# Kernel tuning notes

Measured on AMD Instinct MI355X. Metric: run time of the kernel, lower is better.

The kernel has to match this reference:

```python
import jax, jax.numpy as jnp
import numpy as np

EPS = 1e-5

def _bilinear_sample(xb, ys, xs):
    # xb: [C,H,W]; ys, xs: [H,W] float sample coordinates (zero outside bounds)
    C, H, W = xb.shape
    y0 = jnp.floor(ys); x0 = jnp.floor(xs)
    y1 = y0 + 1.0;      x1 = x0 + 1.0
    wy1 = ys - y0; wy0 = 1.0 - wy1
    wx1 = xs - x0; wx0 = 1.0 - wx1
    def g(yi, xi):
        valid = (yi >= 0) & (yi < H) & (xi >= 0) & (xi < W)
        yc = jnp.clip(yi, 0, H - 1).astype(jnp.int32)
        xc = jnp.clip(xi, 0, W - 1).astype(jnp.int32)
        return xb[:, yc, xc] * valid[None].astype(xb.dtype)  # [C,H,W]
    return (g(y0, x0) * (wy0 * wx0)[None] + g(y0, x1) * (wy0 * wx1)[None]
          + g(y1, x0) * (wy1 * wx0)[None] + g(y1, x1) * (wy1 * wx1)[None])

def _deform_conv2d(x, offset, mask, w, b):
    # x:[B,C,H,W] offset:[B,18,H,W] mask:[B,9,H,W] w:[Co,C,3,3] b:[Co]
    B, C, H, W = x.shape
    Co = w.shape[0]
    ii = jnp.arange(H, dtype=x.dtype)[:, None]
    jj = jnp.arange(W, dtype=x.dtype)[None, :]
    cols = []
    for k in range(9):  # fixed 3x3 kernel positions, row-major (dy=offset[2k], dx=offset[2k+1])
        ky, kx = k // 3 - 1, k % 3 - 1
        ys = ii + ky + offset[:, 2 * k]      # [B,H,W]
        xs = jj + kx + offset[:, 2 * k + 1]
        v = jax.vmap(_bilinear_sample)(x, ys, xs)  # [B,C,H,W]
        cols.append(v * mask[:, k][:, None])
    cols = jnp.stack(cols, axis=1)               # [B,9,C,H,W]
    out = jnp.einsum('bkchw,ock->bohw', cols, w.reshape(Co, C, 9))
    return out + b[None, :, None, None]

def setup_inputs() -> dict:
    key = jax.random.key(0)
    k1, k2, k3, k4 = jax.random.split(key, 4)
    B, Cin, Cout, H, W = 8, 64, 64, 128, 128
    x = jax.random.normal(k1, (B, Cin, H, W), dtype=jnp.float32)
    # offset/mask conv: small weights so learned offsets stay O(1) pixels;
    # bias[18:]=2.0 as in the module's init (masks start near sigmoid(2))
    w_off = jax.random.normal(k2, (27, Cin, 3, 3), dtype=jnp.float32) * 0.01
    b_off = jnp.concatenate([jnp.zeros((18,), jnp.float32), jnp.full((9,), 2.0, jnp.float32)])
    w_dcn = jax.random.normal(k3, (Cout, Cin, 3, 3), dtype=jnp.float32) / np.sqrt(Cin * 9)
    b_dcn = jax.random.normal(k4, (Cout,), dtype=jnp.float32) * 0.01
    return {"x": x, "w_off": w_off, "b_off": b_off, "w_dcn": w_dcn, "b_dcn": b_dcn}

def reference(x, w_off, b_off, w_dcn, b_dcn):
    dn = ('NCHW', 'OIHW', 'NCHW')
    om = jax.lax.conv_general_dilated(x, w_off, (1, 1), 'SAME', dimension_numbers=dn)
    om = om + b_off[None, :, None, None]
    offset = om[:, :18]
    mask = jax.nn.sigmoid(om[:, 18:])
    y = _deform_conv2d(x, offset, mask, w_dcn, b_dcn)
    # InstanceNorm2d (affine=False, biased variance) + ReLU
    mu = jnp.mean(y, axis=(2, 3), keepdims=True)
    var = jnp.var(y, axis=(2, 3), keepdims=True)
    y = (y - mu) * jax.lax.rsqrt(var + EPS)
    return jax.nn.relu(y)
```

## Files before the change

### kernel.cpp

```cpp
#include <hip/hip_runtime.h>
#include <hip/hip_fp16.h>

#define BB   8
#define CIN  64
#define COUT 64
#define HH   128
#define WW   128
#define HWSZ (HH * WW)

typedef _Float16 f16x8 __attribute__((ext_vector_type(8)));
typedef _Float16 h2v   __attribute__((ext_vector_type(2)));
typedef float    f32x4 __attribute__((ext_vector_type(4)));

__device__ __forceinline__ unsigned short f2h_u(float f) {
    __half h = __float2half(f);
    return __half_as_ushort(h);
}
__device__ __forceinline__ unsigned duph(float f) {
    unsigned u = (unsigned)f2h_u(f);
    return u | (u << 16);
}

__device__ __forceinline__ unsigned comb2h(unsigned a, unsigned b, unsigned c, unsigned d,
                                           h2v W0, h2v W1, h2v W2, h2v W3) {
    h2v A = *(h2v*)&a, B = *(h2v*)&b, C = *(h2v*)&c, D = *(h2v*)&d;
    h2v r = A * W0;
    r += B * W1;
    r += C * W2;
    r += D * W3;
    return *(unsigned*)&r;
}


__global__ __launch_bounds__(256) void k_tr(const float* __restrict__ x,
                                            const float* __restrict__ wd,
                                            const float* __restrict__ wof,
                                            unsigned short* __restrict__ xT,
                                            unsigned short* __restrict__ wdT,
                                            unsigned short* __restrict__ wofT,
                                            float4* __restrict__ sums4)
{
    const int t = threadIdx.x;
    const int id = blockIdx.x;
    if (id >= 512) {
        if (id == 512) sums4[t] = make_float4(0.f, 0.f, 0.f, 0.f);
        int base = (id - 512) * 256 + t;
#pragma unroll
        for (int j = 0; j < 4; ++j) {
            int idx = base + j * 16384;
            if (idx < 36864) {
                int k = idx >> 12, rem = idx & 4095, co = rem >> 6, c = rem & 63;
                wdT[idx] = f2h_u(wd[(co * 64 + c) * 9 + k]);
            } else if (idx < 55296) {
                int jj = idx - 36864;
                int k = jj >> 11, rem = jj & 2047, o = rem >> 6, c = rem & 63;
                wofT[jj] = (o < 27) ? f2h_u(wof[(o * 64 + c) * 9 + k]) : 0;
            }
        }
        return;
    }
    __shared__ unsigned short tile[256 * 66];
    const int b = id & 7;
    const int p0 = (id >> 3) * 256;
#pragma unroll
    for (int i = 0; i < 16; ++i) {
        int c = i * 4 + (t >> 6);
        int pl = (t & 63) * 4;
        float4 v = *(const float4*)(x + (((size_t)b * 64 + c) << 14) + p0 + pl);
        tile[(pl + 0) * 66 + c] = f2h_u(v.x);
        tile[(pl + 1) * 66 + c] = f2h_u(v.y);
        tile[(pl + 2) * 66 + c] = f2h_u(v.z);
        tile[(pl + 3) * 66 + c] = f2h_u(v.w);
    }
    __syncthreads();
#pragma unroll
    for (int i = 0; i < 8; ++i) {
        int idd = i * 256 + t;
        int pt = idd >> 3, ck = idd & 7;
        const unsigned* srcp = (const unsigned*)&tile[pt * 66 + ck * 8];
        uint4 r;
        r.x = srcp[0]; r.y = srcp[1]; r.z = srcp[2]; r.w = srcp[3];
        *(uint4*)(xT + ((size_t)b << 20) + ((size_t)(ck >> 2) << 19)
                     + (size_t)(p0 + pt) * 32 + (ck & 3) * 8) = r;
    }
}

__global__ __launch_bounds__(256, 2) void k_off(
    const unsigned short* __restrict__ xT, const unsigned short* __restrict__ wofT,
    const float* __restrict__ bof, float* __restrict__ om)
{
    __shared__ unsigned short tile[8 * 521 * 8];
    const int t = threadIdx.x;
    const int lane = t & 63, wv = t >> 6;
    const int q = lane >> 4, l15 = lane & 15;
    const int b = blockIdx.x & 7;
    const int xblk = blockIdx.x >> 3;
    const int h0 = xblk * 2;
    const int r0 = h0 - 1;
    const unsigned short* xb = xT + ((size_t)b << 20);

#pragma unroll
    for (int i = 0; i < 17; ++i) {
        int id = i * 256 + t;
        if (id < 4160) {
            int m = id & 7, lin = id >> 3;
            int row = lin / 130, col = lin % 130;
            int gy = r0 + row, gx = col - 1;
            uint4 v = {0u, 0u, 0u, 0u};
            if (((unsigned)gy < (unsigned)HH) && ((unsigned)gx < (unsigned)WW))
                v = *(const uint4*)(xb + ((size_t)(m >> 2) << 19)
                                       + (size_t)(gy * WW + gx) * 32 + (m & 3) * 8);
            *(uint4*)&tile[(m * 521 + lin) * 8] = v;
        }
    }
    __syncthreads();

    const int hrow = h0 + (wv >> 1);
    const int c0 = (wv & 1) * 64;

    f32x4 acc[2][4];
#pragma unroll
    for (int mt = 0; mt < 2; ++mt)
#pragma unroll
        for (int nt = 0; nt < 4; ++nt) acc[mt][nt] = (f32x4){0.f, 0.f, 0.f, 0.f};

#pragma unroll
    for (int k = 0; k < 9; ++k) {
        const int ky = k / 3 - 1, kx = k % 3 - 1;
        const int trow = (hrow - h0) + ky + 1;
        const unsigned short* wk = wofT + k * 2048;
#pragma unroll
        for (int ks = 0; ks < 2; ++ks) {
            f16x8 af[2], bfr[4];
#pragma unroll
            for (int mt = 0; mt < 2; ++mt)
                af[mt] = *(const f16x8*)(wk + (mt * 16 + l15) * 64 + ks * 32 + q * 8);
#pragma unroll
            for (int nt = 0; nt < 4; ++nt) {
                int tc = c0 + nt * 16 + l15 + kx + 1;
                bfr[nt] = *(const f16x8*)&tile[((ks * 4 + q) * 521 + trow * 130 + tc) * 8];
            }
#pragma unroll
            for (int mt = 0; mt < 2; ++mt)
#pragma unroll
                for (int nt = 0; nt < 4; ++nt)
                    acc[mt][nt] = __builtin_amdgcn_mfma_f32_16x16x32_f16(
                        af[mt], bfr[nt], acc[mt][nt], 0, 0, 0);
        }
    }

    const int p0 = xblk * 256 + wv * 64;
    float* omb = om + (size_t)b * 27 * HWSZ;
#pragma unroll
    for (int mt = 0; mt < 2; ++mt)
#pragma unroll
        for (int r = 0; r < 4; ++r) {
            int o = mt * 16 + q * 4 + r;
            if (o < 27) {
                float bias = bof[o];
#pragma unroll
                for (int nt = 0; nt < 4; ++nt) {
                    int pp = p0 + nt * 16 + l15;
                    float v = acc[mt][nt][r] + bias;
                    if (o >= 18) v = 1.f / (1.f + __expf(-v));
                    omb[(size_t)o * HWSZ + pp] = v;
                }
            }
        }
}

__global__ __launch_bounds__(256, 2) void k_dcn(
    const unsigned short* __restrict__ xT, const float* __restrict__ om,
    const unsigned short* __restrict__ wdT, const float* __restrict__ bd,
    float* __restrict__ out, float2* __restrict__ sums)
{
    __shared__ unsigned short tile_sh[6 * 128 * 32];
    __shared__ unsigned       adr_sh[4][4][64];
    __shared__ uint4          w_sh[4][64];
    __shared__ float          redS[4][64];
    __shared__ float          redQ[4][64];

    const int t = threadIdx.x;
    const int lane = t & 63, wv = t >> 6;
    const int q = lane >> 4, l15 = lane & 15;
    const int b = blockIdx.x & 7;
    const int pblk = (blockIdx.x >> 3) * 256;
    const int p = pblk + t;
    const int h = p >> 7, w = p & 127;
    const int h0 = pblk >> 7;
    const unsigned short* xbS = xT + ((size_t)b << 20);
    const float* omp = om + (size_t)b * 27 * HWSZ + p;
    const int gch = q * 8;

    f32x4 acc[4][4];
#pragma unroll
    for (int mt = 0; mt < 4; ++mt)
#pragma unroll
        for (int g = 0; g < 4; ++g) acc[mt][g] = (f32x4){0.f, 0.f, 0.f, 0.f};

#define LOADG2(P, g) { \
    if (__builtin_expect((int)(ga[g][0] >> 31), 0)) { \
        P[0] = *(const uint4*)(xbh + (ga[g][0] & 0x7fffffffu) + gch); \
        P[1] = *(const uint4*)(xbh + (ga[g][1] & 0x7fffffffu) + gch); \
        P[2] = *(const uint4*)(xbh + (ga[g][2] & 0x7fffffffu) + gch); \
        P[3] = *(const uint4*)(xbh + (ga[g][3] & 0x7fffffffu) + gch); \
    } else { \
        P[0] = *(const uint4*)&tile_sh[(ga[g][0] & 0x7fffu) + gch]; \
        P[1] = *(const uint4*)&tile_sh[(ga[g][1] & 0x7fffu) + gch]; \
        P[2] = *(const uint4*)&tile_sh[(ga[g][2] & 0x7fffu) + gch]; \
        P[3] = *(const uint4*)&tile_sh[(ga[g][3] & 0x7fffu) + gch]; \
    } }

#define COMB2(DST, P, g) { \
    uint4 pw_ = gw[g]; \
    h2v W0_ = *(h2v*)&pw_.x, W1_ = *(h2v*)&pw_.y; \
    h2v W2_ = *(h2v*)&pw_.z, W3_ = *(h2v*)&pw_.w; \
    uint4 R_; \
    R_.x = comb2h(P[0].x, P[1].x, P[2].x, P[3].x, W0_, W1_, W2_, W3_); \
    R_.y = comb2h(P[0].y, P[1].y, P[2].y, P[3].y, W0_, W1_, W2_, W3_); \
    R_.z = comb2h(P[0].z, P[1].z, P[2].z, P[3].z, W0_, W1_, W2_, W3_); \
    R_.w = comb2h(P[0].w, P[1].w, P[2].w, P[3].w, W0_, W1_, W2_, W3_); \
    DST = *(f16x8*)&R_; }

    for (int hf = 0; hf < 2; ++hf) {
        __syncthreads();
        const unsigned short* xbh = xbS + (hf << 19);
#pragma unroll
        for (int i = 0; i < 12; ++i) {
            int idx = i * 256 + t;
            int s = idx >> 9, u = idx & 511;
            int y = h0 - 2 + s;
            y = min(max(y, 0), HH - 1);
            uint4 v = *(const uint4*)(xbh + (size_t)y * (WW * 32) + u * 8);
            *(uint4*)&tile_sh[idx * 8] = v;
        }
        __syncthreads();

        float offy = omp[0];
        float offx = omp[HWSZ];
        float mk   = omp[18 * HWSZ];

        for (int k = 0; k < 9; ++k) {
            float ys = (float)(h + (k / 3) - 1) + offy;
            float xs = (float)(w + (k % 3) - 1) + offx;
            float fy0 = floorf(ys), fx0 = floorf(xs);
            float wy1 = ys - fy0, wx1 = xs - fx0;
            float wy0 = 1.f - wy1, wx0 = 1.f - wx1;
            int y0 = (int)fy0, x0 = (int)fx0;
            int y1 = y0 + 1, x1 = x0 + 1;
            bool vy0 = (y0 >= 0) && (y0 < HH), vy1 = (y1 >= 0) && (y1 < HH);
            bool vx0 = (x0 >= 0) && (x0 < WW), vx1 = (x1 >= 0) && (x1 < WW);
            int y0c = min(max(y0, 0), HH - 1), y1c = min(max(y1, 0), HH - 1);
            int x0c = min(max(x0, 0), WW - 1), x1c = min(max(x1, 0), WW - 1);
            bool ft = (y0c < h0 - 2) || (y1c > h0 + 3);
            unsigned a0, a1, a2, a3;
            if (!ft) {
                int r0s = (y0c - h0 + 2) * (WW * 32);
                int r1s = (y1c - h0 + 2) * (WW * 32);
                a0 = (unsigned)(r0s + x0c * 32);
                a1 = (unsigned)(r0s + x1c * 32);
                a2 = (unsigned)(r1s + x0c * 32);
                a3 = (unsigned)(r1s + x1c * 32);
            } else {
                unsigned fb = 0x80000000u;
                a0 = fb | (unsigned)((y0c * WW + x0c) * 32);
                a1 = fb | (unsigned)((y0c * WW + x1c) * 32);
                a2 = fb | (unsigned)((y1c * WW + x0c) * 32);
                a3 = fb | (unsigned)((y1c * WW + x1c) * 32);
            }
            adr_sh[wv][0][lane] = a0;
            adr_sh[wv][1][lane] = a1;
            adr_sh[wv][2][lane] = a2;
            adr_sh[wv][3][lane] = a3;
            w_sh[wv][lane] = make_uint4(
                duph((vy0 && vx0) ? mk * wy0 * wx0 : 0.f),
                duph((vy0 && vx1) ? mk * wy0 * wx1 : 0.f),
                duph((vy1 && vx0) ? mk * wy1 * wx0 : 0.f),
                duph((vy1 && vx1) ? mk * wy1 * wx1 : 0.f));
            int kn = (k < 8) ? k + 1 : 8;
            offy = omp[(2 * kn) * HWSZ];
            offx = omp[(2 * kn + 1) * HWSZ];
            mk   = omp[(18 + kn) * HWSZ];
            __builtin_amdgcn_wave_barrier();

            unsigned ga[4][4];
            uint4 gw[4];
#pragma unroll
            for (int g = 0; g < 4; ++g) {
                int pt_ = g * 16 + l15;
                ga[g][0] = adr_sh[wv][0][pt_];
                ga[g][1] = adr_sh[wv][1][pt_];
                ga[g][2] = adr_sh[wv][2][pt_];
                ga[g][3] = adr_sh[wv][3][pt_];
                gw[g] = w_sh[wv][pt_];
            }

            const unsigned short* wk = wdT + k * 4096;
            f16x8 af_[4];
#pragma unroll
            for (int mt = 0; mt < 4; ++mt)
                af_[mt] = *(const f16x8*)(wk + (mt * 16 + l15) * 64 + (hf << 5) + q * 8);

            f16x8 bfr[4];
            uint4 pb[3][4];
            LOADG2(pb[0], 0);
            LOADG2(pb[1], 1);
#pragma unroll
            for (int g = 0; g < 4; ++g) {
                if (g + 2 < 4) LOADG2(pb[(g + 2) % 3], g + 2);
                COMB2(bfr[g], pb[g % 3], g);
            }

#pragma unroll
            for (int mt = 0; mt < 4; ++mt)
#pragma unroll
                for (int g = 0; g < 4; ++g)
                    acc[mt][g] = __builtin_amdgcn_mfma_f32_16x16x32_f16(
                        af_[mt], bfr[g], acc[mt][g], 0, 0, 0);
        }
    }
#undef LOADG2
#undef COMB2

    const int p0 = pblk + wv * 64;
    float* outb = out + (size_t)b * COUT * HWSZ;
#pragma unroll
    for (int mt = 0; mt < 4; ++mt)
#pragma unroll
        for (int r = 0; r < 4; ++r) {
            int co = mt * 16 + q * 4 + r;
            float bias = bd[co];
            float s = 0.f, qq = 0.f;
#pragma unroll
            for (int g = 0; g < 4; ++g) {
                float v = acc[mt][g][r] + bias;
                outb[(size_t)co * HWSZ + p0 + g * 16 + l15] = v;
                s += v; qq += v * v;
            }
#pragma unroll
            for (int m = 1; m < 16; m <<= 1) {
                s += __shfl_xor(s, m);
                qq += __shfl_xor(qq, m);
            }
            if (l15 == 0) { redS[wv][co] = s; redQ[wv][co] = qq; }
        }
    __syncthreads();
    if (t < 64) {
        float S = redS[0][t] + redS[1][t] + redS[2][t] + redS[3][t];
        float Q = redQ[0][t] + redQ[1][t] + redQ[2][t] + redQ[3][t];
        atomicAdd(&sums[b * 64 + t].x, S);
        atomicAdd(&sums[b * 64 + t].y, Q);
    }
}

__global__ __launch_bounds__(256) void k_norm(float* __restrict__ out,
                                              const float2* __restrict__ sums)
{
    const int id = blockIdx.x;
    const int b = id & 7;
    const int rest = id >> 3;
    const int co = rest >> 4;
    const int off = rest & 15;
    const int bco = b * 64 + co;
    const int i = (bco << 12) + off * 256 + threadIdx.x;
    float2 sq = sums[bco];
    float mu  = sq.x * (1.f / (float)HWSZ);
    float var = sq.y * (1.f / (float)HWSZ) - mu * mu;
    float rstd = rsqrtf(var + 1e-5f);
    float4* o4 = (float4*)out;
    float4 v = o4[i];
    v.x = fmaxf((v.x - mu) * rstd, 0.f);
    v.y = fmaxf((v.y - mu) * rstd, 0.f);
    v.z = fmaxf((v.z - mu) * rstd, 0.f);
    v.w = fmaxf((v.w - mu) * rstd, 0.f);
    o4[i] = v;
}

extern "C" void kernel_launch(void* const* d_in, const int* in_sizes, int n_in,
                              void* d_out, int out_size, void* d_ws, size_t ws_size,
                              hipStream_t stream) {
    const float* x   = (const float*)d_in[0];
    const float* wof = (const float*)d_in[1];
    const float* bof = (const float*)d_in[2];
    const float* wd  = (const float*)d_in[3];
    const float* bd  = (const float*)d_in[4];
    float* out = (float*)d_out;

    char* ws = (char*)d_ws;
    unsigned short* xT   = (unsigned short*)ws;
    float*          om   = (float*)(ws + 16777216);
    unsigned short* wdT  = (unsigned short*)(ws + 30932992);
    unsigned short* wofT = (unsigned short*)(ws + 31006720);
    float2*         sums = (float2*)(ws + 31043584);

    k_tr    <<<576, 256, 0, stream>>>(x, wd, wof, xT, wdT, wofT, (float4*)sums);
    k_off   <<<512, 256, 0, stream>>>(xT, wofT, bof, om);
    k_dcn   <<<512, 256, 0, stream>>>(xT, om, wdT, bd, out, sums);
    k_norm  <<<8192, 256, 0, stream>>>(out, (const float2*)sums);
}
```

Baseline: 151.7 us.

## Fuse instance norm into DCN kernel via grid barrier; store offsets/mask as fp16

The separate normalization kernel is removed. After accumulating per-channel sums, each DCN block waits at a global atomic-counter grid barrier, reads the final mean and variance, and writes the normalized, ReLU'd output straight from its accumulators. This avoids writing the 32 MB fp32 output and reading it back. The offset/mask tensor is also stored in fp16 to halve its traffic. The barrier is only safe if all 512 blocks are co-resident (2 per CU on 256 CUs), otherwise it can deadlock, and fp16 offsets lose some precision.

```diff
diff --git a/kernel.cpp b/kernel.cpp
--- a/kernel.cpp
+++ b/kernel.cpp
@@ -15,6 +15,10 @@
 __device__ __forceinline__ unsigned short f2h_u(float f) {
     __half h = __float2half(f);
     return __half_as_ushort(h);
+}
+__device__ __forceinline__ float h2f_u(unsigned short u) {
+    _Float16 f = *(_Float16*)&u;
+    return (float)f;
 }
 __device__ __forceinline__ unsigned duph(float f) {
     unsigned u = (unsigned)f2h_u(f);
@@ -38,12 +42,16 @@
                                             unsigned short* __restrict__ xT,
                                             unsigned short* __restrict__ wdT,
                                             unsigned short* __restrict__ wofT,
-                                            float4* __restrict__ sums4)
+                                            float4* __restrict__ sums4,
+                                            unsigned* __restrict__ ctr)
 {
     const int t = threadIdx.x;
     const int id = blockIdx.x;
     if (id >= 512) {
-        if (id == 512) sums4[t] = make_float4(0.f, 0.f, 0.f, 0.f);
+        if (id == 512) {
+            sums4[t] = make_float4(0.f, 0.f, 0.f, 0.f);
+            if (t == 0) *ctr = 0;
+        }
         int base = (id - 512) * 256 + t;
 #pragma unroll
         for (int j = 0; j < 4; ++j) {
@@ -87,7 +95,7 @@
 
 __global__ __launch_bounds__(256, 2) void k_off(
     const unsigned short* __restrict__ xT, const unsigned short* __restrict__ wofT,
-    const float* __restrict__ bof, float* __restrict__ om)
+    const float* __restrict__ bof, unsigned short* __restrict__ om)
 {
     __shared__ unsigned short tile[8 * 521 * 8];
     const int t = threadIdx.x;
@@ -150,7 +158,7 @@
     }
 
     const int p0 = xblk * 256 + wv * 64;
-    float* omb = om + (size_t)b * 27 * HWSZ;
+    unsigned short* omb = om + (size_t)b * 27 * HWSZ;
 #pragma unroll
     for (int mt = 0; mt < 2; ++mt)
 #pragma unroll
@@ -163,16 +171,17 @@
                     int pp = p0 + nt * 16 + l15;
                     float v = acc[mt][nt][r] + bias;
                     if (o >= 18) v = 1.f / (1.f + __expf(-v));
-                    omb[(size_t)o * HWSZ + pp] = v;
+                    omb[(size_t)o * HWSZ + pp] = f2h_u(v);
                 }
             }
         }
 }
 
 __global__ __launch_bounds__(256, 2) void k_dcn(
-    const unsigned short* __restrict__ xT, const float* __restrict__ om,
+    const unsigned short* __restrict__ xT, const unsigned short* __restrict__ om,
     const unsigned short* __restrict__ wdT, const float* __restrict__ bd,
-    float* __restrict__ out, float2* __restrict__ sums)
+    float* __restrict__ out, float2* __restrict__ sums,
+    unsigned* __restrict__ ctr)
 {
     __shared__ unsigned short tile_sh[6 * 128 * 32];
     __shared__ unsigned       adr_sh[4][4][64];
@@ -189,7 +198,7 @@
     const int h = p >> 7, w = p & 127;
     const int h0 = pblk >> 7;
     const unsigned short* xbS = xT + ((size_t)b << 20);
-    const float* omp = om + (size_t)b * 27 * HWSZ + p;
+    const unsigned short* omp = om + (size_t)b * 27 * HWSZ + p;
     const int gch = q * 8;
 
     f32x4 acc[4][4];
@@ -236,9 +245,9 @@
         }
         __syncthreads();
 
-        float offy = omp[0];
-        float offx = omp[HWSZ];
-        float mk   = omp[18 * HWSZ];
+        float offy = h2f_u(omp[0]);
+        float offx = h2f_u(omp[HWSZ]);
+        float mk   = h2f_u(omp[18 * HWSZ]);
 
         for (int k = 0; k < 9; ++k) {
             float ys = (float)(h + (k / 3) - 1) + offy;
@@ -278,9 +287,9 @@
                 duph((vy1 && vx0) ? mk * wy1 * wx0 : 0.f),
                 duph((vy1 && vx1) ? mk * wy1 * wx1 : 0.f));
             int kn = (k < 8) ? k + 1 : 8;
-            offy = omp[(2 * kn) * HWSZ];
-            offx = omp[(2 * kn + 1) * HWSZ];
-            mk   = omp[(18 + kn) * HWSZ];
+            offy = h2f_u(omp[(2 * kn) * HWSZ]);
+            offx = h2f_u(omp[(2 * kn + 1) * HWSZ]);
+            mk   = h2f_u(omp[(18 + kn) * HWSZ]);
             __builtin_amdgcn_wave_barrier();
 
             unsigned ga[4][4];
@@ -322,8 +331,6 @@
 #undef LOADG2
 #undef COMB2
 
-    const int p0 = pblk + wv * 64;
-    float* outb = out + (size_t)b * COUT * HWSZ;
 #pragma unroll
     for (int mt = 0; mt < 4; ++mt)
 #pragma unroll
@@ -334,7 +341,6 @@
 #pragma unroll
             for (int g = 0; g < 4; ++g) {
                 float v = acc[mt][g][r] + bias;
-                outb[(size_t)co * HWSZ + p0 + g * 16 + l15] = v;
                 s += v; qq += v * v;
             }
 #pragma unroll
@@ -350,30 +356,45 @@
         float Q = redQ[0][t] + redQ[1][t] + redQ[2][t] + redQ[3][t];
         atomicAdd(&sums[b * 64 + t].x, S);
         atomicAdd(&sums[b * 64 + t].y, Q);
-    }
-}
-
-__global__ __launch_bounds__(256) void k_norm(float* __restrict__ out,
-                                              const float2* __restrict__ sums)
-{
-    const int id = blockIdx.x;
-    const int b = id & 7;
-    const int rest = id >> 3;
-    const int co = rest >> 4;
-    const int off = rest & 15;
-    const int bco = b * 64 + co;
-    const int i = (bco << 12) + off * 256 + threadIdx.x;
-    float2 sq = sums[bco];
-    float mu  = sq.x * (1.f / (float)HWSZ);
-    float var = sq.y * (1.f / (float)HWSZ) - mu * mu;
-    float rstd = rsqrtf(var + 1e-5f);
-    float4* o4 = (float4*)out;
-    float4 v = o4[i];
-    v.x = fmaxf((v.x - mu) * rstd, 0.f);
-    v.y = fmaxf((v.y - mu) * rstd, 0.f);
-    v.z = fmaxf((v.z - mu) * rstd, 0.f);
-    v.w = fmaxf((v.w - mu) * rstd, 0.f);
-    o4[i] = v;
+        __threadfence();
+    }
+    __syncthreads();
+    if (t == 0) {
+        __hip_atomic_fetch_add(ctr, 1u, __ATOMIC_ACQ_REL, __HIP_MEMORY_SCOPE_AGENT);
+        while (__hip_atomic_load(ctr, __ATOMIC_ACQUIRE, __HIP_MEMORY_SCOPE_AGENT) < 512u)
+            __builtin_amdgcn_s_sleep(8);
+    }
+    __syncthreads();
+
+    if (t < 64) {
+        float S = __hip_atomic_load(&sums[b * 64 + t].x, __ATOMIC_RELAXED,
+                                    __HIP_MEMORY_SCOPE_AGENT);
+        float Q = __hip_atomic_load(&sums[b * 64 + t].y, __ATOMIC_RELAXED,
+                                    __HIP_MEMORY_SCOPE_AGENT);
+        float mu  = S * (1.f / (float)HWSZ);
+        float var = Q * (1.f / (float)HWSZ) - mu * mu;
+        redS[0][t] = mu;
+        redQ[0][t] = rsqrtf(var + 1e-5f);
+    }
+    __syncthreads();
+
+    const int p0w = pblk + wv * 64;
+    float* outb = out + (size_t)b * COUT * HWSZ;
+#pragma unroll
+    for (int mt = 0; mt < 4; ++mt)
+#pragma unroll
+        for (int r = 0; r < 4; ++r) {
+            int co = mt * 16 + q * 4 + r;
+            float mu   = redS[0][co];
+            float rstd = redQ[0][co];
+            float bias = bd[co];
+#pragma unroll
+            for (int g = 0; g < 4; ++g) {
+                float v = acc[mt][g][r] + bias;
+                v = fmaxf((v - mu) * rstd, 0.f);
+                __builtin_nontemporal_store(v, &outb[(size_t)co * HWSZ + p0w + g * 16 + l15]);
+            }
+        }
 }
 
 extern "C" void kernel_launch(void* const* d_in, const int* in_sizes, int n_in,
@@ -388,13 +409,13 @@
 
     char* ws = (char*)d_ws;
     unsigned short* xT   = (unsigned short*)ws;
-    float*          om   = (float*)(ws + 16777216);
-    unsigned short* wdT  = (unsigned short*)(ws + 30932992);
-    unsigned short* wofT = (unsigned short*)(ws + 31006720);
-    float2*         sums = (float2*)(ws + 31043584);
-
-    k_tr    <<<576, 256, 0, stream>>>(x, wd, wof, xT, wdT, wofT, (float4*)sums);
+    unsigned short* om   = (unsigned short*)(ws + 16777216);
+    unsigned short* wdT  = (unsigned short*)(ws + 23855104);
+    unsigned short* wofT = (unsigned short*)(ws + 23928832);
+    float2*         sums = (float2*)(ws + 23965696);
+    unsigned*       ctr  = (unsigned*)(ws + 23969792);
+
+    k_tr    <<<576, 256, 0, stream>>>(x, wd, wof, xT, wdT, wofT, (float4*)sums, ctr);
     k_off   <<<512, 256, 0, stream>>>(xT, wofT, bof, om);
-    k_dcn   <<<512, 256, 0, stream>>>(xT, om, wdT, bd, out, sums);
-    k_norm  <<<8192, 256, 0, stream>>>(out, (const float2*)sums);
-}
+    k_dcn   <<<512, 256, 0, stream>>>(xT, om, wdT, bd, out, sums, ctr);
+}
```

Result: slower. 206.2 us (+35.9%).
